# Optimization experiments

Measured on AMD Instinct MI355X. Metric: run time of the kernel, lower is better.

The kernel has to match this reference:

```python
import jax, jax.numpy as jnp
import numpy as np

B, S, E, H = 2, 2048, 1024, 16
D = E // H  # head_dim = 64


def setup_inputs() -> dict:
    key = jax.random.key(0)
    k1, k2, k3 = jax.random.split(key, 3)
    scale = 0.02  # GPT-2 init scale
    return {
        "hidden_states": jax.random.normal(k1, (B, S, E), dtype=jnp.float32),
        "c_attn_w": jax.random.normal(k2, (E, 3 * E), dtype=jnp.float32) * scale,
        "c_attn_b": jnp.zeros((3 * E,), dtype=jnp.float32),
        "c_proj_w": jax.random.normal(k3, (E, E), dtype=jnp.float32) * scale,
        "c_proj_b": jnp.zeros((E,), dtype=jnp.float32),
    }


def reference(hidden_states, c_attn_w, c_attn_b, c_proj_w, c_proj_b):
    # Conv1D: x @ W + b  -> qkv [B, S, 3E]
    qkv = hidden_states @ c_attn_w + c_attn_b
    q, k, v = jnp.split(qkv, 3, axis=-1)

    # split heads -> [B, H, S, D]
    def split_heads(t):
        return t.reshape(B, S, H, D).transpose(0, 2, 1, 3)

    q, k, v = split_heads(q), split_heads(k), split_heads(v)

    # naive full attention: QK^T / sqrt(D) -> softmax -> @ V
    attn_weights = jnp.einsum("bhqd,bhkd->bhqk", q, k) / jnp.sqrt(
        jnp.asarray(D, dtype=q.dtype)
    )
    attn_weights = jax.nn.softmax(attn_weights, axis=-1)
    attn_output = jnp.einsum("bhqk,bhkd->bhqd", attn_weights, v)

    # merge heads -> [B, S, E], then output projection
    attn_output = attn_output.transpose(0, 2, 1, 3).reshape(B, S, E)
    attn_output = attn_output @ c_proj_w + c_proj_b
    return attn_output
```

## Files before the change

kernel.cpp:

```cpp
#include <hip/hip_runtime.h>

#define SEQ 2048
#define EMB 1024
#define KDIM 1024
#define CF 0.180336880111113f

typedef __attribute__((ext_vector_type(8))) short short8_t;
typedef __attribute__((ext_vector_type(4))) float floatx4;
typedef __attribute__((ext_vector_type(4))) unsigned short ushort4_t;

#define GLOAD16(gp, lp)                                                        \
  __builtin_amdgcn_global_load_lds(                                            \
      (const __attribute__((address_space(1))) void*)(gp),                     \
      (__attribute__((address_space(3))) void*)(lp), 16, 0, 0)

#define WGBAR()                                   \
  do {                                            \
    __asm__ __volatile__("" ::: "memory");        \
    __builtin_amdgcn_s_barrier();                 \
    __asm__ __volatile__("" ::: "memory");        \
  } while (0)

static __device__ __forceinline__ unsigned short f2bf(float x) {
  unsigned int u = __float_as_uint(x);
  return (unsigned short)((u + 0x7fffu + ((u >> 16) & 1u)) >> 16);
}

__global__ __launch_bounds__(256) void conv_bf(
    const float* __restrict__ X, unsigned short* __restrict__ Y, int n4) {
  int i = blockIdx.x * 256 + threadIdx.x;
  if (i >= n4) return;
  float4 v = *(const float4*)&X[(size_t)i * 4];
  ushort4_t h = {f2bf(v.x), f2bf(v.y), f2bf(v.z), f2bf(v.w)};
  *(ushort4_t*)&Y[(size_t)i * 4] = h;
}

__global__ __launch_bounds__(256) void tconv(
    const float* __restrict__ W, unsigned short* __restrict__ T, int N, int K) {
  __shared__ float Tl[64][65];
  const int tid = threadIdx.x, lx = tid & 15, ly = tid >> 4;
  const int n0 = blockIdx.x * 64, k0 = blockIdx.y * 64;
#pragma unroll
  for (int u = 0; u < 4; ++u) {
    int r = u * 16 + ly;
    float4 v = *(const float4*)&W[(size_t)(k0 + r) * N + n0 + lx * 4];
    Tl[r][lx * 4 + 0] = v.x;
    Tl[r][lx * 4 + 1] = v.y;
    Tl[r][lx * 4 + 2] = v.z;
    Tl[r][lx * 4 + 3] = v.w;
  }
  __syncthreads();
#pragma unroll
  for (int u = 0; u < 4; ++u) {
    int n = u * 16 + ly;
    ushort4_t h;
#pragma unroll
    for (int v = 0; v < 4; ++v) h[v] = f2bf(Tl[lx * 4 + v][n]);
    *(ushort4_t*)&T[(size_t)(n0 + n) * K + k0 + lx * 4] = h;
  }
}

template <int MODE, int BN>
__global__ __launch_bounds__(256) void gemm_bf(
    const unsigned short* __restrict__ Ag, const unsigned short* __restrict__ Bg,
    const float* __restrict__ bias, float* __restrict__ outF,
    unsigned short* __restrict__ qk, unsigned short* __restrict__ vt, int N) {
  __shared__ __attribute__((aligned(16))) unsigned short Ah[128 * 64];
  __shared__ __attribute__((aligned(16))) unsigned short Bh[BN * 64];
  const int NJ = BN / 32;

  const int tid = threadIdx.x;
  const int w = tid >> 6, lane = tid & 63;
  const int quad = lane >> 4, c = lane & 15;
  const int bm = blockIdx.y * 128, bn = blockIdx.x * BN;
  const int wm = (w >> 1) * 64, wn = (w & 1) * (BN / 2);

  const unsigned short* gsrc = (w < 2) ? Ag : Bg;
  unsigned short* ldst = (w < 2) ? (Ah + (w & 1) * 64 * 64) : (Bh + (w & 1) * (BN / 2) * 64);
  const int rbase = (w < 2) ? (bm + (w & 1) * 64) : (bn + (w & 1) * (BN / 2));
  const int nloads = (w < 2) ? 8 : (BN / 16);
  const int srow = lane >> 3;
  const int sblk = (lane & 7) ^ srow;
  const char* gp0 = (const char*)(gsrc + (size_t)(rbase + srow) * KDIM) + sblk * 16;

  floatx4 acc[4][NJ];
  const floatx4 z = {0.f, 0.f, 0.f, 0.f};
#pragma unroll
  for (int i = 0; i < 4; ++i)
#pragma unroll
    for (int j = 0; j < NJ; ++j) acc[i][j] = z;

  const int rk = c & 7;

  for (int k0 = 0; k0 < KDIM; k0 += 64) {
    __syncthreads();
    const char* gp = gp0 + k0 * 2;
    for (int i = 0; i < nloads; ++i) GLOAD16(gp + (size_t)i * 8 * (KDIM * 2), &ldst[i * 512]);
    __syncthreads();

#pragma unroll
    for (int kq = 0; kq < 2; ++kq) {
      const int oct = ((4 * kq + quad) ^ rk) * 8;
      short8_t a[4], b[NJ];
#pragma unroll
      for (int i = 0; i < 4; ++i)
        a[i] = *(const short8_t*)&Ah[(wm + 16 * i + c) * 64 + oct];
#pragma unroll
      for (int j = 0; j < NJ; ++j)
        b[j] = *(const short8_t*)&Bh[(wn + 16 * j + c) * 64 + oct];
#pragma unroll
      for (int i = 0; i < 4; ++i)
#pragma unroll
        for (int j = 0; j < NJ; ++j)
          acc[i][j] = __builtin_amdgcn_mfma_f32_16x16x32_bf16(a[i], b[j], acc[i][j], 0, 0, 0);
    }
  }

#pragma unroll
  for (int i = 0; i < 4; ++i) {
    const int r0 = bm + wm + 16 * i + quad * 4;
#pragma unroll
    for (int j = 0; j < NJ; ++j) {
      const int col = bn + wn + 16 * j + c;
      const float bv = bias[col];
      float v0 = acc[i][j][0] + bv, v1 = acc[i][j][1] + bv;
      float v2 = acc[i][j][2] + bv, v3 = acc[i][j][3] + bv;
      if (MODE == 0) {
        if (col < 1024) { v0 *= CF; v1 *= CF; v2 *= CF; v3 *= CF; }
        if (bn < 2048) {
          qk[(size_t)(r0 + 0) * 2048 + col] = f2bf(v0);
          qk[(size_t)(r0 + 1) * 2048 + col] = f2bf(v1);
          qk[(size_t)(r0 + 2) * 2048 + col] = f2bf(v2);
          qk[(size_t)(r0 + 3) * 2048 + col] = f2bf(v3);
        } else {
          const int c2 = col - 2048, hh = c2 >> 6, d = c2 & 63;
          const int bb = r0 >> 11, s = r0 & 2047;
          ushort4_t pk = {f2bf(v0), f2bf(v1), f2bf(v2), f2bf(v3)};
          *(ushort4_t*)&vt[((size_t)(bb * 16 + hh) * 64 + d) * 2048 + s] = pk;
        }
      } else {
        outF[(size_t)(r0 + 0) * N + col] = v0;
        outF[(size_t)(r0 + 1) * N + col] = v1;
        outF[(size_t)(r0 + 2) * N + col] = v2;
        outF[(size_t)(r0 + 3) * N + col] = v3;
      }
    }
  }
}

static __device__ __forceinline__ void stage_kv(
    int w, int srow, int sblkg, const unsigned short* __restrict__ gK,
    const unsigned short* __restrict__ gV, unsigned short* Kbuf,
    unsigned short* Vbuf, int jt) {
  if (w < 2) {
    const unsigned short* g0 = gK + (size_t)(jt * 64 + w * 32 + srow) * 2048 + sblkg * 8;
    unsigned short* l0 = &Kbuf[(w * 32) * 64];
#pragma unroll
    for (int i = 0; i < 4; ++i) GLOAD16(g0 + (size_t)i * 8 * 2048, &l0[i * 512]);
  } else {
    const unsigned short* g0 = gV + (size_t)((w - 2) * 32 + srow) * 2048 + jt * 64 + sblkg * 8;
    unsigned short* l0 = &Vbuf[((w - 2) * 32) * 64];
#pragma unroll
    for (int i = 0; i < 4; ++i) GLOAD16(g0 + (size_t)i * 8 * 2048, &l0[i * 512]);
  }
}

__global__ __launch_bounds__(256) void attn4(
    const unsigned short* __restrict__ qk, const unsigned short* __restrict__ vt,
    unsigned short* __restrict__ ao) {
  __shared__ __attribute__((aligned(16))) unsigned short Ks[2][64 * 64];
  __shared__ __attribute__((aligned(16))) unsigned short Vs[2][64 * 64];
  __shared__ __attribute__((aligned(16))) unsigned short Ps[4][32 * 64];

  const int tid = threadIdx.x;
  const int w = tid >> 6, lane = tid & 63, quad = lane >> 4, c = lane & 15;
  const int q0 = blockIdx.x * 128, h = blockIdx.y, b = blockIdx.z;
  const int rk = c & 7;

  short8_t qf[2][2];
  {
    const size_t rb = (size_t)b * SEQ + q0 + w * 32;
#pragma unroll
    for (int mi = 0; mi < 2; ++mi) {
      const size_t qr = (rb + mi * 16 + c) * 2048 + h * 64 + quad * 8;
      qf[mi][0] = *(const short8_t*)&qk[qr];
      qf[mi][1] = *(const short8_t*)&qk[qr + 32];
    }
  }
  __asm__ __volatile__("s_waitcnt vmcnt(0)" ::: "memory");

  floatx4 O[2][4], Osum[2];
  const floatx4 z = {0.f, 0.f, 0.f, 0.f};
#pragma unroll
  for (int mi = 0; mi < 2; ++mi) {
    Osum[mi] = z;
#pragma unroll
    for (int dg = 0; dg < 4; ++dg) O[mi][dg] = z;
  }
  short8_t ones;
#pragma unroll
  for (int e = 0; e < 8; ++e) ones[e] = (short)0x3F80;

  const int srow = lane >> 3;
  const int sblkg = (lane & 7) ^ srow;
  const unsigned short* gK = qk + (size_t)b * SEQ * 2048 + 1024 + h * 64;
  const unsigned short* gV = vt + (size_t)(b * 16 + h) * 64 * 2048;
  unsigned short* myPs = Ps[w];

  stage_kv(w, srow, sblkg, gK, gV, Ks[0], Vs[0], 0);

  for (int t = 0; t < 32; ++t) {
    const int cur = t & 1;
    WGBAR();
    stage_kv(w, srow, sblkg, gK, gV, Ks[cur ^ 1], Vs[cur ^ 1], (t + 1) & 31);
    __asm__ __volatile__("s_waitcnt vmcnt(4)" ::: "memory");
    WGBAR();
    const unsigned short* Kc = Ks[cur];
    const unsigned short* Vc = Vs[cur];

    floatx4 S[2][4];
#pragma unroll
    for (int mi = 0; mi < 2; ++mi)
#pragma unroll
      for (int jg = 0; jg < 4; ++jg) S[mi][jg] = z;
#pragma unroll
    for (int kd = 0; kd < 2; ++kd) {
      const int oct = ((4 * kd + quad) ^ rk) * 8;
#pragma unroll
      for (int jg = 0; jg < 4; ++jg) {
        short8_t kf = *(const short8_t*)&Kc[(jg * 16 + c) * 64 + oct];
#pragma unroll
        for (int mi = 0; mi < 2; ++mi)
          S[mi][jg] = __builtin_amdgcn_mfma_f32_16x16x32_bf16(kf, qf[mi][kd], S[mi][jg], 0, 0, 0);
      }
    }

#pragma unroll
    for (int mi = 0; mi < 2; ++mi) {
      const int qrow = (mi * 16 + c) * 64;
#pragma unroll
      for (int jg = 0; jg < 4; ++jg) {
        float p0 = __builtin_amdgcn_exp2f(S[mi][jg][0]);
        float p1 = __builtin_amdgcn_exp2f(S[mi][jg][1]);
        float p2 = __builtin_amdgcn_exp2f(S[mi][jg][2]);
        float p3 = __builtin_amdgcn_exp2f(S[mi][jg][3]);
        unsigned int pk01 = (__float_as_uint(p1) & 0xFFFF0000u) | (__float_as_uint(p0) >> 16);
        unsigned int pk23 = (__float_as_uint(p3) & 0xFFFF0000u) | (__float_as_uint(p2) >> 16);
        const int jp0 = 8 * jg + 2 * quad;
#pragma unroll
        for (int u = 0; u < 2; ++u) {
          const int jp = jp0 + u;
          const int off = ((jp >> 2) ^ rk) * 8 + (jp & 3) * 2;
          *(unsigned int*)&myPs[qrow + off] = u ? pk23 : pk01;
        }
      }
    }
    __asm__ __volatile__("s_waitcnt lgkmcnt(0)" ::: "memory");

#pragma unroll
    for (int kq = 0; kq < 2; ++kq) {
      const int oct = ((4 * kq + quad) ^ rk) * 8;
      short8_t pb[2];
#pragma unroll
      for (int mi = 0; mi < 2; ++mi) {
        pb[mi] = *(const short8_t*)&myPs[(mi * 16 + c) * 64 + oct];
        Osum[mi] = __builtin_amdgcn_mfma_f32_16x16x32_bf16(ones, pb[mi], Osum[mi], 0, 0, 0);
      }
#pragma unroll
      for (int dg = 0; dg < 4; ++dg) {
        short8_t vf = *(const short8_t*)&Vc[(dg * 16 + c) * 64 + oct];
#pragma unroll
        for (int mi = 0; mi < 2; ++mi)
          O[mi][dg] = __builtin_amdgcn_mfma_f32_16x16x32_bf16(vf, pb[mi], O[mi][dg], 0, 0, 0);
      }
    }
  }

  __asm__ __volatile__("s_waitcnt vmcnt(0)" ::: "memory");

#pragma unroll
  for (int mi = 0; mi < 2; ++mi) {
    const float inv = 1.0f / Osum[mi][0];
    const size_t row = (size_t)b * SEQ + q0 + w * 32 + mi * 16 + c;
#pragma unroll
    for (int dg = 0; dg < 4; ++dg) {
      ushort4_t ov = {f2bf(O[mi][dg][0] * inv), f2bf(O[mi][dg][1] * inv),
                      f2bf(O[mi][dg][2] * inv), f2bf(O[mi][dg][3] * inv)};
      *(ushort4_t*)&ao[row * EMB + h * 64 + dg * 16 + quad * 4] = ov;
    }
  }
}

extern "C" void kernel_launch(void* const* d_in, const int* in_sizes, int n_in,
                              void* d_out, int out_size, void* d_ws, size_t ws_size,
                              hipStream_t stream) {
  const float* hs = (const float*)d_in[0];
  const float* c_attn_w = (const float*)d_in[1];
  const float* c_attn_b = (const float*)d_in[2];
  const float* c_proj_w = (const float*)d_in[3];
  const float* c_proj_b = (const float*)d_in[4];
  float* out = (float*)d_out;

  char* ws = (char*)d_ws;
  unsigned short* hsb = (unsigned short*)(ws + 0);
  unsigned short* qk  = (unsigned short*)(ws + 8388608);
  unsigned short* vt  = (unsigned short*)(ws + 25165824);
  unsigned short* aob = (unsigned short*)(ws + 33554432);
  unsigned short* w1t = (unsigned short*)(ws + 41943040);
  unsigned short* w2t = (unsigned short*)(ws + 48234496);

  conv_bf<<<4096, 256, 0, stream>>>(hs, hsb, (2 * SEQ * EMB) / 4);
  tconv<<<dim3(48, 16), 256, 0, stream>>>(c_attn_w, w1t, 3 * EMB, EMB);
  tconv<<<dim3(16, 16), 256, 0, stream>>>(c_proj_w, w2t, EMB, EMB);
  gemm_bf<0, 128><<<dim3(24, 32), 256, 0, stream>>>(hsb, w1t, c_attn_b, nullptr, qk, vt, 3 * EMB);
  attn4<<<dim3(16, 16, 2), 256, 0, stream>>>(qk, vt, aob);
  gemm_bf<1, 64><<<dim3(16, 32), 256, 0, stream>>>(aob, w2t, c_proj_b, out, nullptr, nullptr, EMB);
}
```

Measured before the change: 197.6 us.

## Split attention KV range across blocks and vectorize GEMM epilogues

```diff
diff --git a/kernel.cpp b/kernel.cpp
--- a/kernel.cpp
+++ b/kernel.cpp
@@ -24,6 +24,9 @@
 static __device__ __forceinline__ unsigned short f2bf(float x) {
   unsigned int u = __float_as_uint(x);
   return (unsigned short)((u + 0x7fffu + ((u >> 16) & 1u)) >> 16);
+}
+static __device__ __forceinline__ float bf2f(unsigned short h) {
+  return __uint_as_float(((unsigned int)h) << 16);
 }
 
 __global__ __launch_bounds__(256) void conv_bf(
@@ -64,7 +67,8 @@
 __global__ __launch_bounds__(256) void gemm_bf(
     const unsigned short* __restrict__ Ag, const unsigned short* __restrict__ Bg,
     const float* __restrict__ bias, float* __restrict__ outF,
-    unsigned short* __restrict__ qk, unsigned short* __restrict__ vt, int N) {
+    unsigned short* __restrict__ qk, unsigned short* __restrict__ vt,
+    int colbase) {
   __shared__ __attribute__((aligned(16))) unsigned short Ah[128 * 64];
   __shared__ __attribute__((aligned(16))) unsigned short Bh[BN * 64];
   const int NJ = BN / 32;
@@ -72,7 +76,7 @@
   const int tid = threadIdx.x;
   const int w = tid >> 6, lane = tid & 63;
   const int quad = lane >> 4, c = lane & 15;
-  const int bm = blockIdx.y * 128, bn = blockIdx.x * BN;
+  const int bm = blockIdx.y * 128, bn = colbase + blockIdx.x * BN;
   const int wm = (w >> 1) * 64, wn = (w & 1) * (BN / 2);
 
   const unsigned short* gsrc = (w < 2) ? Ag : Bg;
@@ -111,75 +115,86 @@
 #pragma unroll
       for (int i = 0; i < 4; ++i)
 #pragma unroll
-        for (int j = 0; j < NJ; ++j)
-          acc[i][j] = __builtin_amdgcn_mfma_f32_16x16x32_bf16(a[i], b[j], acc[i][j], 0, 0, 0);
-    }
-  }
-
-#pragma unroll
-  for (int i = 0; i < 4; ++i) {
-    const int r0 = bm + wm + 16 * i + quad * 4;
-#pragma unroll
-    for (int j = 0; j < NJ; ++j) {
-      const int col = bn + wn + 16 * j + c;
-      const float bv = bias[col];
-      float v0 = acc[i][j][0] + bv, v1 = acc[i][j][1] + bv;
-      float v2 = acc[i][j][2] + bv, v3 = acc[i][j][3] + bv;
-      if (MODE == 0) {
-        if (col < 1024) { v0 *= CF; v1 *= CF; v2 *= CF; v3 *= CF; }
-        if (bn < 2048) {
-          qk[(size_t)(r0 + 0) * 2048 + col] = f2bf(v0);
-          qk[(size_t)(r0 + 1) * 2048 + col] = f2bf(v1);
-          qk[(size_t)(r0 + 2) * 2048 + col] = f2bf(v2);
-          qk[(size_t)(r0 + 3) * 2048 + col] = f2bf(v3);
+        for (int j = 0; j < NJ; ++j) {
+          if (MODE == 1)
+            acc[i][j] = __builtin_amdgcn_mfma_f32_16x16x32_bf16(a[i], b[j], acc[i][j], 0, 0, 0);
+          else
+            acc[i][j] = __builtin_amdgcn_mfma_f32_16x16x32_bf16(b[j], a[i], acc[i][j], 0, 0, 0);
+        }
+    }
+  }
+
+  if (MODE == 1) {
+#pragma unroll
+    for (int i = 0; i < 4; ++i) {
+      const int r0 = bm + wm + 16 * i + quad * 4;
+#pragma unroll
+      for (int j = 0; j < NJ; ++j) {
+        const int col = bn + wn + 16 * j + c;
+        const float bv = bias[col];
+        const int c2 = col - 2048, hh = c2 >> 6, d = c2 & 63;
+        const int bb = r0 >> 11, s = r0 & 2047;
+        ushort4_t pk = {f2bf(acc[i][j][0] + bv), f2bf(acc[i][j][1] + bv),
+                        f2bf(acc[i][j][2] + bv), f2bf(acc[i][j][3] + bv)};
+        *(ushort4_t*)&vt[((size_t)(bb * 16 + hh) * 64 + d) * 2048 + s] = pk;
+      }
+    }
+  } else {
+#pragma unroll
+    for (int i = 0; i < 4; ++i) {
+      const int row = bm + wm + 16 * i + c;
+#pragma unroll
+      for (int j = 0; j < NJ; ++j) {
+        const int col0 = bn + wn + 16 * j + quad * 4;
+        floatx4 v = acc[i][j] + *(const floatx4*)&bias[col0];
+        if (MODE == 0) {
+          if (col0 < 1024) v = v * CF;
+          ushort4_t pk = {f2bf(v[0]), f2bf(v[1]), f2bf(v[2]), f2bf(v[3])};
+          *(ushort4_t*)&qk[(size_t)row * 2048 + col0] = pk;
         } else {
-          const int c2 = col - 2048, hh = c2 >> 6, d = c2 & 63;
-          const int bb = r0 >> 11, s = r0 & 2047;
-          ushort4_t pk = {f2bf(v0), f2bf(v1), f2bf(v2), f2bf(v3)};
-          *(ushort4_t*)&vt[((size_t)(bb * 16 + hh) * 64 + d) * 2048 + s] = pk;
+          *(floatx4*)&outF[(size_t)row * 1024 + col0] = v;
         }
-      } else {
-        outF[(size_t)(r0 + 0) * N + col] = v0;
-        outF[(size_t)(r0 + 1) * N + col] = v1;
-        outF[(size_t)(r0 + 2) * N + col] = v2;
-        outF[(size_t)(r0 + 3) * N + col] = v3;
-      }
-    }
-  }
-}
-
-static __device__ __forceinline__ void stage_kv(
+      }
+    }
+  }
+}
+
+static __device__ __forceinline__ void stage_kv8(
     int w, int srow, int sblkg, const unsigned short* __restrict__ gK,
     const unsigned short* __restrict__ gV, unsigned short* Kbuf,
     unsigned short* Vbuf, int jt) {
-  if (w < 2) {
-    const unsigned short* g0 = gK + (size_t)(jt * 64 + w * 32 + srow) * 2048 + sblkg * 8;
-    unsigned short* l0 = &Kbuf[(w * 32) * 64];
-#pragma unroll
-    for (int i = 0; i < 4; ++i) GLOAD16(g0 + (size_t)i * 8 * 2048, &l0[i * 512]);
+  if (w < 4) {
+    const unsigned short* g0 = gK + (size_t)(jt * 64 + w * 16 + srow) * 2048 + sblkg * 8;
+    unsigned short* l0 = &Kbuf[(w * 16) * 64];
+#pragma unroll
+    for (int i = 0; i < 2; ++i) GLOAD16(g0 + (size_t)i * 8 * 2048, &l0[i * 512]);
   } else {
-    const unsigned short* g0 = gV + (size_t)((w - 2) * 32 + srow) * 2048 + jt * 64 + sblkg * 8;
-    unsigned short* l0 = &Vbuf[((w - 2) * 32) * 64];
-#pragma unroll
-    for (int i = 0; i < 4; ++i) GLOAD16(g0 + (size_t)i * 8 * 2048, &l0[i * 512]);
-  }
-}
-
-__global__ __launch_bounds__(256) void attn4(
+    const unsigned short* g0 = gV + (size_t)((w - 4) * 16 + srow) * 2048 + jt * 64 + sblkg * 8;
+    unsigned short* l0 = &Vbuf[((w - 4) * 16) * 64];
+#pragma unroll
+    for (int i = 0; i < 2; ++i) GLOAD16(g0 + (size_t)i * 8 * 2048, &l0[i * 512]);
+  }
+}
+
+__global__ __launch_bounds__(512) void attn5(
     const unsigned short* __restrict__ qk, const unsigned short* __restrict__ vt,
-    unsigned short* __restrict__ ao) {
+    unsigned short* __restrict__ ph0, unsigned short* __restrict__ ph1,
+    float* __restrict__ lsum) {
   __shared__ __attribute__((aligned(16))) unsigned short Ks[2][64 * 64];
   __shared__ __attribute__((aligned(16))) unsigned short Vs[2][64 * 64];
-  __shared__ __attribute__((aligned(16))) unsigned short Ps[4][32 * 64];
+  __shared__ __attribute__((aligned(16))) unsigned short Ps[8][32 * 64];
 
   const int tid = threadIdx.x;
   const int w = tid >> 6, lane = tid & 63, quad = lane >> 4, c = lane & 15;
-  const int q0 = blockIdx.x * 128, h = blockIdx.y, b = blockIdx.z;
+  const int h = blockIdx.y;
+  const int b = blockIdx.z >> 1, half = blockIdx.z & 1;
+  const int q0 = blockIdx.x * 256 + w * 32;
+  const int tstart = half * 16;
   const int rk = c & 7;
 
   short8_t qf[2][2];
   {
-    const size_t rb = (size_t)b * SEQ + q0 + w * 32;
+    const size_t rb = (size_t)b * SEQ + q0;
 #pragma unroll
     for (int mi = 0; mi < 2; ++mi) {
       const size_t qr = (rb + mi * 16 + c) * 2048 + h * 64 + quad * 8;
@@ -207,13 +222,13 @@
   const unsigned short* gV = vt + (size_t)(b * 16 + h) * 64 * 2048;
   unsigned short* myPs = Ps[w];
 
-  stage_kv(w, srow, sblkg, gK, gV, Ks[0], Vs[0], 0);
-
-  for (int t = 0; t < 32; ++t) {
+  stage_kv8(w, srow, sblkg, gK, gV, Ks[0], Vs[0], tstart);
+
+  for (int t = 0; t < 16; ++t) {
     const int cur = t & 1;
     WGBAR();
-    stage_kv(w, srow, sblkg, gK, gV, Ks[cur ^ 1], Vs[cur ^ 1], (t + 1) & 31);
-    __asm__ __volatile__("s_waitcnt vmcnt(4)" ::: "memory");
+    stage_kv8(w, srow, sblkg, gK, gV, Ks[cur ^ 1], Vs[cur ^ 1], tstart + ((t + 1) & 15));
+    __asm__ __volatile__("s_waitcnt vmcnt(2)" ::: "memory");
     WGBAR();
     const unsigned short* Kc = Ks[cur];
     const unsigned short* Vc = Vs[cur];
@@ -278,17 +293,38 @@
 
   __asm__ __volatile__("s_waitcnt vmcnt(0)" ::: "memory");
 
+  unsigned short* ph = half ? ph1 : ph0;
 #pragma unroll
   for (int mi = 0; mi < 2; ++mi) {
-    const float inv = 1.0f / Osum[mi][0];
-    const size_t row = (size_t)b * SEQ + q0 + w * 32 + mi * 16 + c;
+    const size_t row = (size_t)b * SEQ + q0 + mi * 16 + c;
 #pragma unroll
     for (int dg = 0; dg < 4; ++dg) {
-      ushort4_t ov = {f2bf(O[mi][dg][0] * inv), f2bf(O[mi][dg][1] * inv),
-                      f2bf(O[mi][dg][2] * inv), f2bf(O[mi][dg][3] * inv)};
-      *(ushort4_t*)&ao[row * EMB + h * 64 + dg * 16 + quad * 4] = ov;
-    }
-  }
+      ushort4_t ov = {f2bf(O[mi][dg][0]), f2bf(O[mi][dg][1]),
+                      f2bf(O[mi][dg][2]), f2bf(O[mi][dg][3])};
+      *(ushort4_t*)&ph[row * EMB + h * 64 + dg * 16 + quad * 4] = ov;
+    }
+    if (quad == 0)
+      lsum[((size_t)(half * 2 + b) * 16 + h) * 2048 + q0 + mi * 16 + c] = Osum[mi][0];
+  }
+}
+
+__global__ __launch_bounds__(256) void combine(
+    const unsigned short* __restrict__ p0, const unsigned short* __restrict__ p1,
+    const float* __restrict__ lsum, unsigned short* __restrict__ aob) {
+  const int i = blockIdx.x * 256 + threadIdx.x;
+  const size_t base = (size_t)i * 4;
+  const int e = (int)(base & (EMB - 1));
+  const size_t row = base >> 10;
+  const int b = (int)(row >> 11), s = (int)(row & 2047), h = e >> 6;
+  const float l0 = lsum[((size_t)(0 + b) * 16 + h) * 2048 + s];
+  const float l1 = lsum[((size_t)(2 + b) * 16 + h) * 2048 + s];
+  const float inv = 1.0f / (l0 + l1);
+  ushort4_t a = *(const ushort4_t*)&p0[base];
+  ushort4_t d = *(const ushort4_t*)&p1[base];
+  ushort4_t o;
+#pragma unroll
+  for (int k = 0; k < 4; ++k) o[k] = f2bf((bf2f(a[k]) + bf2f(d[k])) * inv);
+  *(ushort4_t*)&aob[base] = o;
 }
 
 extern "C" void kernel_launch(void* const* d_in, const int* in_sizes, int n_in,
@@ -305,14 +341,18 @@
   unsigned short* hsb = (unsigned short*)(ws + 0);
   unsigned short* qk  = (unsigned short*)(ws + 8388608);
   unsigned short* vt  = (unsigned short*)(ws + 25165824);
-  unsigned short* aob = (unsigned short*)(ws + 33554432);
+  unsigned short* ph0 = (unsigned short*)(ws + 33554432);
   unsigned short* w1t = (unsigned short*)(ws + 41943040);
   unsigned short* w2t = (unsigned short*)(ws + 48234496);
+  float*          lsum = (float*)(ws + 50331648);
+  unsigned short* ph1 = hsb;
 
   conv_bf<<<4096, 256, 0, stream>>>(hs, hsb, (2 * SEQ * EMB) / 4);
   tconv<<<dim3(48, 16), 256, 0, stream>>>(c_attn_w, w1t, 3 * EMB, EMB);
   tconv<<<dim3(16, 16), 256, 0, stream>>>(c_proj_w, w2t, EMB, EMB);
-  gemm_bf<0, 128><<<dim3(24, 32), 256, 0, stream>>>(hsb, w1t, c_attn_b, nullptr, qk, vt, 3 * EMB);
-  attn4<<<dim3(16, 16, 2), 256, 0, stream>>>(qk, vt, aob);
-  gemm_bf<1, 64><<<dim3(16, 32), 256, 0, stream>>>(aob, w2t, c_proj_b, out, nullptr, nullptr, EMB);
-}
+  gemm_bf<0, 128><<<dim3(16, 32), 256, 0, stream>>>(hsb, w1t, c_attn_b, nullptr, qk, nullptr, 0);
+  gemm_bf<1, 128><<<dim3(8, 32), 256, 0, stream>>>(hsb, w1t, c_attn_b, nullptr, nullptr, vt, 2048);
+  attn5<<<dim3(8, 16, 4), 512, 0, stream>>>(qk, vt, ph0, ph1, lsum);
+  combine<<<4096, 256, 0, stream>>>(ph0, ph1, lsum, ph0);
+  gemm_bf<2, 64><<<dim3(16, 32), 256, 0, stream>>>(ph0, w2t, c_proj_b, out, nullptr, nullptr, 0);
+}
```

Result: slower. 208.9 us (+5.7%).
